# Kernel tuning notes

Hardware: AMD Instinct MI355X
Metric: run time of the kernel (lower is better)

The kernel has to match this reference:

```python
import jax, jax.numpy as jnp
import numpy as np

N_EMBD = 256
N_HEAD = 8
BATCH = 4
SEQ = 2048
NEG_BIAS = -1000000000.0


def setup_inputs() -> dict:
    key = jax.random.key(0)
    ks = jax.random.split(key, 5)
    scale = 1.0 / np.sqrt(N_EMBD)
    x = jax.random.normal(ks[0], (BATCH, SEQ, N_EMBD), dtype=jnp.float32)
    # torch Linear weight layout: (out_features, in_features)
    Wq = jax.random.normal(ks[1], (N_EMBD * N_HEAD, N_EMBD), dtype=jnp.float32) * scale
    Wk = jax.random.normal(ks[2], (N_EMBD * N_HEAD, N_EMBD), dtype=jnp.float32) * scale
    Wv = jax.random.normal(ks[3], (N_EMBD * N_HEAD, N_EMBD), dtype=jnp.float32) * scale
    Wo = jax.random.normal(ks[4], (N_EMBD, N_EMBD * N_HEAD), dtype=jnp.float32) * scale / np.sqrt(N_HEAD)
    return {"x": x, "Wq": Wq, "Wk": Wk, "Wv": Wv, "Wo": Wo}


def reference(x, Wq, Wk, Wv, Wo):
    B, L, E = x.shape
    H, D = N_HEAD, N_EMBD  # d_head == n_embd in this module
    # projections: x @ W.T, then split heads -> (B, H, L, D)
    def proj(W):
        y = jnp.einsum('ble,fe->blf', x, W)  # (B, L, H*D)
        return y.reshape(B, L, H, D).transpose(0, 2, 1, 3)
    q, k, v = proj(Wq), proj(Wk), proj(Wv)
    scores = jnp.einsum('bhld,bhmd->bhlm', q, k) * (E ** -0.5)
    # first (non-causal) softmax over full rows
    attn = jax.nn.softmax(scores, axis=-1)
    # causal mask replaces disallowed probs with large negative bias, then softmax again
    causal = jnp.tril(jnp.ones((L, L), dtype=bool))
    attn = jnp.where(causal[None, None], attn, jnp.asarray(NEG_BIAS, attn.dtype))
    attn = jax.nn.softmax(attn, axis=-1)
    out = jnp.einsum('bhlm,bhmd->bhld', attn, v)  # (B, H, L, D)
    out = out.transpose(0, 2, 1, 3).reshape(B, L, H * D)
    return jnp.einsum('blf,ef->ble', out, Wo)  # (B, L, E)
```

## Files before the change

kernel.cpp:

```cpp
#include <hip/hip_runtime.h>
#include <stdint.h>

typedef unsigned short ushort_t;
typedef __attribute__((ext_vector_type(8))) short bf16x8;
typedef __attribute__((ext_vector_type(4))) float f32x4;
typedef __attribute__((ext_vector_type(4))) unsigned short us4;

#define DEV __device__ __forceinline__

DEV ushort_t f2bf(float f) {
    unsigned int u = __float_as_uint(f);
    u += 0x7fffu + ((u >> 16) & 1u);
    return (ushort_t)(u >> 16);
}

DEV void async16(const ushort_t* g, ushort_t* l) {
    __builtin_amdgcn_global_load_lds(
        (const __attribute__((address_space(1))) void*)g,
        (__attribute__((address_space(3))) void*)l,
        16, 0, 0);
}

__global__ void convert_kernel(const float* __restrict__ x, const float* __restrict__ wq,
                               const float* __restrict__ wk, const float* __restrict__ wv,
                               const float* __restrict__ wo,
                               ushort_t* __restrict__ xb, ushort_t* __restrict__ wqb,
                               ushort_t* __restrict__ wkb, ushort_t* __restrict__ wvb,
                               ushort_t* __restrict__ wob)
{
    const int i = blockIdx.x * 256 + threadIdx.x;
    const float* src; ushort_t* dst; int off;
    if (i < 524288)      { src = x;  dst = xb;  off = i; }
    else if (i < 655360) { src = wq; dst = wqb; off = i - 524288; }
    else if (i < 786432) { src = wk; dst = wkb; off = i - 655360; }
    else if (i < 917504) { src = wv; dst = wvb; off = i - 786432; }
    else                 { src = wo; dst = wob; off = i - 917504; }
    const float4 v = ((const float4*)src)[off];
    us4 o;
    o[0] = f2bf(v.x); o[1] = f2bf(v.y); o[2] = f2bf(v.z); o[3] = f2bf(v.w);
    ((us4*)dst)[off] = o;
}

__global__ __launch_bounds__(256, 2) void qkv_gemm_kernel(
    const ushort_t* __restrict__ A, const ushort_t* __restrict__ wq,
    const ushort_t* __restrict__ wk, const ushort_t* __restrict__ wv,
    ushort_t* __restrict__ q_out, ushort_t* __restrict__ k_out,
    ushort_t* __restrict__ vt_out)
{
    __shared__ ushort_t At[128 * 64];
    __shared__ ushort_t Bt[128 * 64];

    const int K = 256, N = 2048;
    const int z = blockIdx.z;
    const ushort_t* Bm = (z == 0) ? wq : (z == 1) ? wk : wv;

    const int tid  = threadIdx.x;
    const int wave = tid >> 6;
    const int lane = tid & 63;
    const int quad = lane >> 4;
    const int l15  = lane & 15;
    const int mhalf = wave >> 1;
    const int nhalf = wave & 1;
    const int m0 = blockIdx.x * 128;
    const int n0 = blockIdx.y * 128;

    f32x4 acc[4][4];
#pragma unroll
    for (int mf = 0; mf < 4; ++mf)
#pragma unroll
        for (int nf = 0; nf < 4; ++nf)
#pragma unroll
            for (int r = 0; r < 4; ++r) acc[mf][nf][r] = 0.f;

    const int crow = (lane & 7) ^ (lane >> 3);

    for (int k0 = 0; k0 < K; k0 += 64) {
        __syncthreads();
#pragma unroll
        for (int t = 0; t < 4; ++t) {
            const int row = wave * 32 + t * 8 + (lane >> 3);
            async16(A + (size_t)(m0 + row) * K + k0 + crow * 8,
                    At + (wave * 32 + t * 8) * 64 + lane * 8);
            async16(Bm + (size_t)(n0 + row) * K + k0 + crow * 8,
                    Bt + (wave * 32 + t * 8) * 64 + lane * 8);
        }
        __syncthreads();
#pragma unroll
        for (int ks = 0; ks < 2; ++ks) {
            bf16x8 af[4], bf[4];
#pragma unroll
            for (int mf = 0; mf < 4; ++mf) {
                const int ml = mhalf * 64 + mf * 16 + l15;
                const int c = (ks * 4 + quad) ^ (ml & 7);
                af[mf] = *(const bf16x8*)(At + ml * 64 + c * 8);
            }
#pragma unroll
            for (int nf = 0; nf < 4; ++nf) {
                const int nl = nhalf * 64 + nf * 16 + l15;
                const int c = (ks * 4 + quad) ^ (nl & 7);
                bf[nf] = *(const bf16x8*)(Bt + nl * 64 + c * 8);
            }
#pragma unroll
            for (int mf = 0; mf < 4; ++mf)
#pragma unroll
                for (int nf = 0; nf < 4; ++nf)
                    acc[mf][nf] = __builtin_amdgcn_mfma_f32_16x16x32_bf16(
                        af[mf], bf[nf], acc[mf][nf], 0, 0, 0);
        }
    }

    if (z == 2) {
#pragma unroll
        for (int mf = 0; mf < 4; ++mf)
#pragma unroll
            for (int nf = 0; nf < 4; ++nf) {
                const int row = m0 + mhalf * 64 + mf * 16 + quad * 4;
                const int col = n0 + nhalf * 64 + nf * 16 + l15;
                const int b_ = row >> 11, l_ = row & 2047;
                const int h_ = col >> 8, d_ = col & 255;
                us4 pk;
#pragma unroll
                for (int r = 0; r < 4; ++r) pk[r] = f2bf(acc[mf][nf][r]);
                *(us4*)(vt_out + (((size_t)(b_ * 8 + h_) * 256 + d_) * 2048 + l_)) = pk;
            }
    } else {
        ushort_t* Cout = z ? k_out : q_out;
        const float sc = z ? 1.0f : 0.0625f;
#pragma unroll
        for (int mf = 0; mf < 4; ++mf)
#pragma unroll
            for (int nf = 0; nf < 4; ++nf)
#pragma unroll
                for (int r = 0; r < 4; ++r) {
                    const int row = m0 + mhalf * 64 + mf * 16 + quad * 4 + r;
                    const int col = n0 + nhalf * 64 + nf * 16 + l15;
                    Cout[(size_t)row * N + col] = f2bf(acc[mf][nf][r] * sc);
                }
    }
}

__global__ __launch_bounds__(256, 2) void out_gemm_splitk_kernel(
    const ushort_t* __restrict__ A, const ushort_t* __restrict__ Bm,
    float* __restrict__ Pout, int M, int N, int K)
{
    __shared__ ushort_t At[128 * 64];
    __shared__ ushort_t Bt[128 * 64];

    const int tid  = threadIdx.x;
    const int wave = tid >> 6;
    const int lane = tid & 63;
    const int quad = lane >> 4;
    const int l15  = lane & 15;
    const int mhalf = wave >> 1;
    const int nhalf = wave & 1;
    const int m0 = blockIdx.x * 128;
    const int n0 = blockIdx.y * 128;
    const int ks0 = blockIdx.z * 512;

    f32x4 acc[4][4];
#pragma unroll
    for (int mf = 0; mf < 4; ++mf)
#pragma unroll
        for (int nf = 0; nf < 4; ++nf)
#pragma unroll
            for (int r = 0; r < 4; ++r) acc[mf][nf][r] = 0.f;

    const int crow = (lane & 7) ^ (lane >> 3);

    for (int k0 = ks0; k0 < ks0 + 512; k0 += 64) {
        __syncthreads();
#pragma unroll
        for (int t = 0; t < 4; ++t) {
            const int row = wave * 32 + t * 8 + (lane >> 3);
            async16(A + (size_t)(m0 + row) * K + k0 + crow * 8,
                    At + (wave * 32 + t * 8) * 64 + lane * 8);
            async16(Bm + (size_t)(n0 + row) * K + k0 + crow * 8,
                    Bt + (wave * 32 + t * 8) * 64 + lane * 8);
        }
        __syncthreads();
#pragma unroll
        for (int ks = 0; ks < 2; ++ks) {
            bf16x8 af[4], bf[4];
#pragma unroll
            for (int mf = 0; mf < 4; ++mf) {
                const int ml = mhalf * 64 + mf * 16 + l15;
                const int c = (ks * 4 + quad) ^ (ml & 7);
                af[mf] = *(const bf16x8*)(At + ml * 64 + c * 8);
            }
#pragma unroll
            for (int nf = 0; nf < 4; ++nf) {
                const int nl = nhalf * 64 + nf * 16 + l15;
                const int c = (ks * 4 + quad) ^ (nl & 7);
                bf[nf] = *(const bf16x8*)(Bt + nl * 64 + c * 8);
            }
#pragma unroll
            for (int mf = 0; mf < 4; ++mf)
#pragma unroll
                for (int nf = 0; nf < 4; ++nf)
                    acc[mf][nf] = __builtin_amdgcn_mfma_f32_16x16x32_bf16(
                        af[mf], bf[nf], acc[mf][nf], 0, 0, 0);
        }
    }

    float* Cp = Pout + (size_t)blockIdx.z * M * N;
#pragma unroll
    for (int mf = 0; mf < 4; ++mf)
#pragma unroll
        for (int nf = 0; nf < 4; ++nf)
#pragma unroll
            for (int r = 0; r < 4; ++r) {
                const int row = m0 + mhalf * 64 + mf * 16 + quad * 4 + r;
                const int col = n0 + nhalf * 64 + nf * 16 + l15;
                Cp[(size_t)row * N + col] = acc[mf][nf][r];
            }
}

__global__ void reduce4_kernel(const float4* __restrict__ p, float4* __restrict__ out)
{
    const int i = blockIdx.x * 256 + threadIdx.x;
    float4 a = p[i];
    const float4 b = p[i + 524288];
    const float4 c = p[i + 1048576];
    const float4 d = p[i + 1572864];
    a.x += b.x + c.x + d.x;
    a.y += b.y + c.y + d.y;
    a.z += b.z + c.z + d.z;
    a.w += b.w + c.w + d.w;
    out[i] = a;
}

__global__ __launch_bounds__(256, 2) void out_gemm_kernel(
    const ushort_t* __restrict__ A, const ushort_t* __restrict__ Bm,
    float* __restrict__ Cout, int M, int N, int K)
{
    __shared__ ushort_t At[128 * 64];
    __shared__ ushort_t Bt[128 * 64];

    const int tid  = threadIdx.x;
    const int wave = tid >> 6;
    const int lane = tid & 63;
    const int quad = lane >> 4;
    const int l15  = lane & 15;
    const int mhalf = wave >> 1;
    const int nhalf = wave & 1;
    const int m0 = blockIdx.x * 128;
    const int n0 = blockIdx.y * 128;

    f32x4 acc[4][4];
#pragma unroll
    for (int mf = 0; mf < 4; ++mf)
#pragma unroll
        for (int nf = 0; nf < 4; ++nf)
#pragma unroll
            for (int r = 0; r < 4; ++r) acc[mf][nf][r] = 0.f;

    const int crow = (lane & 7) ^ (lane >> 3);

    for (int k0 = 0; k0 < K; k0 += 64) {
        __syncthreads();
#pragma unroll
        for (int t = 0; t < 4; ++t) {
            const int row = wave * 32 + t * 8 + (lane >> 3);
            async16(A + (size_t)(m0 + row) * K + k0 + crow * 8,
                    At + (wave * 32 + t * 8) * 64 + lane * 8);
            async16(Bm + (size_t)(n0 + row) * K + k0 + crow * 8,
                    Bt + (wave * 32 + t * 8) * 64 + lane * 8);
        }
        __syncthreads();
#pragma unroll
        for (int ks = 0; ks < 2; ++ks) {
            bf16x8 af[4], bf[4];
#pragma unroll
            for (int mf = 0; mf < 4; ++mf) {
                const int ml = mhalf * 64 + mf * 16 + l15;
                const int c = (ks * 4 + quad) ^ (ml & 7);
                af[mf] = *(const bf16x8*)(At + ml * 64 + c * 8);
            }
#pragma unroll
            for (int nf = 0; nf < 4; ++nf) {
                const int nl = nhalf * 64 + nf * 16 + l15;
                const int c = (ks * 4 + quad) ^ (nl & 7);
                bf[nf] = *(const bf16x8*)(Bt + nl * 64 + c * 8);
            }
#pragma unroll
            for (int mf = 0; mf < 4; ++mf)
#pragma unroll
                for (int nf = 0; nf < 4; ++nf)
                    acc[mf][nf] = __builtin_amdgcn_mfma_f32_16x16x32_bf16(
                        af[mf], bf[nf], acc[mf][nf], 0, 0, 0);
        }
    }

#pragma unroll
    for (int mf = 0; mf < 4; ++mf)
#pragma unroll
        for (int nf = 0; nf < 4; ++nf)
#pragma unroll
            for (int r = 0; r < 4; ++r) {
                const int row = m0 + mhalf * 64 + mf * 16 + quad * 4 + r;
                const int col = n0 + nhalf * 64 + nf * 16 + l15;
                Cout[(size_t)row * N + col] = acc[mf][nf][r];
            }
}

__global__ __launch_bounds__(512, 4) void pass1_kernel(
    const ushort_t* __restrict__ q_ws, const ushort_t* __restrict__ k_ws,
    float* __restrict__ rz_ws)
{
    __shared__ ushort_t Kt[128 * 256];
    __shared__ float zred[2][128];

    const int tid  = threadIdx.x;
    const int wave = tid >> 6;
    const int lane = tid & 63;
    const int quad = lane >> 4;
    const int l15  = lane & 15;
    const int iq    = wave >> 1;
    const int jhalf = wave & 1;

    const int g  = blockIdx.x;
    const int h  = g & 7;
    const int b  = (g >> 3) & 3;
    const int it = g >> 5;
    const int bh = b * 8 + h;
    const int i0 = it * 128;

    const size_t qkbase = (size_t)b * 2048 * 2048 + (size_t)h * 256;

    bf16x8 qf[2][8];
#pragma unroll
    for (int ng = 0; ng < 2; ++ng) {
        const int i_l = iq * 32 + ng * 16 + l15;
        const ushort_t* qr = q_ws + qkbase + (size_t)(i0 + i_l) * 2048;
#pragma unroll
        for (int ks = 0; ks < 8; ++ks)
            qf[ng][ks] = *(const bf16x8*)(qr + ks * 32 + quad * 8);
    }

    float z[2] = {0.f, 0.f};

    for (int jt = 0; jt < 16; ++jt) {
        __syncthreads();
        {
            const ushort_t* kb = k_ws + qkbase + (size_t)jt * 128 * 2048;
#pragma unroll
            for (int t = 0; t < 8; ++t) {
                const int row = wave * 16 + t * 2 + (lane >> 5);
                const int c = (lane & 31) ^ (row & 7);
                async16(kb + (size_t)row * 2048 + c * 8,
                        Kt + (wave * 16 + t * 2) * 256 + lane * 8);
            }
        }
        __syncthreads();

#pragma unroll
        for (int jh = 0; jh < 2; ++jh) {
            f32x4 sacc[2][2];
#pragma unroll
            for (int a = 0; a < 2; ++a)
#pragma unroll
                for (int c = 0; c < 2; ++c)
#pragma unroll
                    for (int r = 0; r < 4; ++r) sacc[a][c][r] = 0.f;

            __builtin_amdgcn_s_setprio(1);
#pragma unroll
            for (int ks = 0; ks < 8; ++ks) {
                bf16x8 af[2];
#pragma unroll
                for (int mg = 0; mg < 2; ++mg) {
                    const int j_l = jh * 64 + jhalf * 32 + mg * 16 + l15;
                    const int c = (ks * 4 + quad) ^ (j_l & 7);
                    af[mg] = *(const bf16x8*)(Kt + j_l * 256 + c * 8);
                }
#pragma unroll
                for (int mg = 0; mg < 2; ++mg)
#pragma unroll
                    for (int ng = 0; ng < 2; ++ng)
                        sacc[mg][ng] = __builtin_amdgcn_mfma_f32_16x16x32_bf16(
                            af[mg], qf[ng][ks], sacc[mg][ng], 0, 0, 0);
            }
            __builtin_amdgcn_s_setprio(0);

#pragma unroll
            for (int ng = 0; ng < 2; ++ng)
#pragma unroll
                for (int mg = 0; mg < 2; ++mg)
#pragma unroll
                    for (int r = 0; r < 4; ++r)
                        z[ng] += __expf(sacc[mg][ng][r]);
        }
    }

#pragma unroll
    for (int ng = 0; ng < 2; ++ng) {
        z[ng] += __shfl_xor(z[ng], 16);
        z[ng] += __shfl_xor(z[ng], 32);
    }
    __syncthreads();
    if (quad == 0) {
#pragma unroll
        for (int ng = 0; ng < 2; ++ng) {
            const int i_l = iq * 32 + ng * 16 + l15;
            zred[jhalf][i_l] = z[ng];
        }
    }
    __syncthreads();
    if (tid < 128)
        rz_ws[(size_t)bh * 2048 + i0 + tid] = 1.0f / (zred[0][tid] + zred[1][tid]);
}

__global__ __launch_bounds__(512, 2) void pass2_kernel(
    const ushort_t* __restrict__ q_ws, const ushort_t* __restrict__ k_ws,
    const ushort_t* __restrict__ vt_ws, const float* __restrict__ rz_ws,
    ushort_t* __restrict__ attn_out)
{
    __shared__ ushort_t smem[40960];
    ushort_t* Kt = smem;
    ushort_t* Vt = smem + 16384;
    ushort_t* Wt = smem + 32768;

    const int tid  = threadIdx.x;
    const int wave = tid >> 6;
    const int lane = tid & 63;
    const int quad = lane >> 4;
    const int l15  = lane & 15;
    const int iq    = wave >> 1;
    const int jhalf = wave & 1;

    const int g  = blockIdx.x;
    const int h  = g & 7;
    const int b  = (g >> 3) & 3;
    const int x  = g >> 5;
    const int it = (x < 8) ? (2 * x) : (31 - 2 * x);
    const int bh = b * 8 + h;
    const int i0 = it * 128;

    const size_t qkbase = (size_t)b * 2048 * 2048 + (size_t)h * 256;

    bf16x8 qf[2][8];
#pragma unroll
    for (int ng = 0; ng < 2; ++ng) {
        const int i_l = iq * 32 + ng * 16 + l15;
        const ushort_t* qr = q_ws + qkbase + (size_t)(i0 + i_l) * 2048;
#pragma unroll
        for (int ks = 0; ks < 8; ++ks)
            qf[ng][ks] = *(const bf16x8*)(qr + ks * 32 + quad * 8);
    }

    float rzrow[2];
#pragma unroll
    for (int ng = 0; ng < 2; ++ng) {
        const int i_l = iq * 32 + ng * 16 + l15;
        rzrow[ng] = rz_ws[(size_t)bh * 2048 + i0 + i_l];
    }

    f32x4 oacc[2][8];
#pragma unroll
    for (int mg = 0; mg < 2; ++mg)
#pragma unroll
        for (int nf = 0; nf < 8; ++nf)
#pragma unroll
            for (int r = 0; r < 4; ++r) oacc[mg][nf][r] = 0.f;
    float den[2] = {0.f, 0.f};

    const int jmax = 2 * it + 1;
    for (int jt = 0; jt <= jmax; ++jt) {
        const int j0 = jt * 64;
        const int jzone = jt - 2 * it;
        __syncthreads();
        {
            const ushort_t* kb = k_ws + qkbase + (size_t)j0 * 2048;
#pragma unroll
            for (int t = 0; t < 4; ++t) {
                const int row = wave * 8 + t * 2 + (lane >> 5);
                const int c = (lane & 31) ^ (row & 7);
                async16(kb + (size_t)row * 2048 + c * 8,
                        Kt + (wave * 8 + t * 2) * 256 + lane * 8);
            }
            const ushort_t* vb = vt_ws + (size_t)bh * 256 * 2048 + j0;
#pragma unroll
            for (int t = 0; t < 4; ++t) {
                const int row = wave * 32 + t * 8 + (lane >> 3);
                const int c = (lane & 7) ^ (row & 7);
                async16(vb + (size_t)row * 2048 + c * 8,
                        Vt + (wave * 32 + t * 8) * 64 + lane * 8);
            }
        }
        __syncthreads();

        f32x4 sacc[2][2];
#pragma unroll
        for (int a = 0; a < 2; ++a)
#pragma unroll
            for (int c = 0; c < 2; ++c)
#pragma unroll
                for (int r = 0; r < 4; ++r) sacc[a][c][r] = 0.f;

#pragma unroll
        for (int ks = 0; ks < 8; ++ks) {
            bf16x8 af[2];
#pragma unroll
            for (int mg = 0; mg < 2; ++mg) {
                const int j_l = jhalf * 32 + mg * 16 + l15;
                const int c = (ks * 4 + quad) ^ (j_l & 7);
                af[mg] = *(const bf16x8*)(Kt + j_l * 256 + c * 8);
            }
#pragma unroll
            for (int mg = 0; mg < 2; ++mg)
#pragma unroll
                for (int ng = 0; ng < 2; ++ng)
                    sacc[mg][ng] = __builtin_amdgcn_mfma_f32_16x16x32_bf16(
                        af[mg], qf[ng][ks], sacc[mg][ng], 0, 0, 0);
        }

#pragma unroll
        for (int mg = 0; mg < 2; ++mg) {
#pragma unroll
            for (int ng = 0; ng < 2; ++ng) {
                const int i_l = iq * 32 + ng * 16 + l15;
                const int jb = jhalf * 32 + mg * 16 + quad * 4;
                us4 wp;
#pragma unroll
                for (int r = 0; r < 4; ++r) {
                    const float p = __expf(sacc[mg][ng][r]) * rzrow[ng];
                    float w = __expf(p);
                    if (jzone >= 0 && (jzone * 64 + jb + r > i_l)) w = 0.f;
                    den[ng] += w;
                    wp[r] = f2bf(w);
                }
                const int c = (jb >> 3) ^ (i_l & 7);
                *(us4*)(Wt + i_l * 64 + c * 8 + (jb & 7)) = wp;
            }
        }
        __syncthreads();

#pragma unroll
        for (int ks = 0; ks < 2; ++ks) {
            bf16x8 aw[2];
#pragma unroll
            for (int mg = 0; mg < 2; ++mg) {
                const int i_l = iq * 32 + mg * 16 + l15;
                const int c = (ks * 4 + quad) ^ (i_l & 7);
                aw[mg] = *(const bf16x8*)(Wt + i_l * 64 + c * 8);
            }
#pragma unroll
            for (int nf = 0; nf < 8; ++nf) {
                const int d = jhalf * 128 + nf * 16 + l15;
                const int c = (ks * 4 + quad) ^ (d & 7);
                const bf16x8 bv = *(const bf16x8*)(Vt + d * 64 + c * 8);
                oacc[0][nf] = __builtin_amdgcn_mfma_f32_16x16x32_bf16(aw[0], bv, oacc[0][nf], 0, 0, 0);
                oacc[1][nf] = __builtin_amdgcn_mfma_f32_16x16x32_bf16(aw[1], bv, oacc[1][nf], 0, 0, 0);
            }
        }
    }

    __syncthreads();
    {
        float* dbuf = (float*)Kt;
#pragma unroll
        for (int ng = 0; ng < 2; ++ng) {
            const int i_l = iq * 32 + ng * 16 + l15;
            dbuf[(jhalf * 4 + quad) * 128 + i_l] = den[ng];
        }
    }
    __syncthreads();
    if (tid < 128) {
        const float* dbuf = (const float*)Kt;
        float s = 0.f;
#pragma unroll
        for (int p = 0; p < 8; ++p) s += dbuf[p * 128 + tid];
        ((float*)Kt)[1024 + tid] = 1.0f / s;
    }
    __syncthreads();
    {
        const float* rden = (const float*)Kt + 1024;
#pragma unroll
        for (int mg = 0; mg < 2; ++mg) {
#pragma unroll
            for (int r = 0; r < 4; ++r) {
                const int i_l = iq * 32 + mg * 16 + quad * 4 + r;
                const float rd = rden[i_l];
                ushort_t* orow = attn_out + qkbase + (size_t)(i0 + i_l) * 2048;
#pragma unroll
                for (int nf = 0; nf < 8; ++nf) {
                    const int d = jhalf * 128 + nf * 16 + l15;
                    orow[d] = f2bf(oacc[mg][nf][r] * rd);
                }
            }
        }
    }
}

extern "C" void kernel_launch(void* const* d_in, const int* in_sizes, int n_in,
                              void* d_out, int out_size, void* d_ws, size_t ws_size,
                              hipStream_t stream) {
    const float* x  = (const float*)d_in[0];
    const float* Wq = (const float*)d_in[1];
    const float* Wk = (const float*)d_in[2];
    const float* Wv = (const float*)d_in[3];
    const float* Wo = (const float*)d_in[4];

    char* ws = (char*)d_ws;
    ushort_t* xb    = (ushort_t*)(ws);
    ushort_t* wqb   = (ushort_t*)(ws + 4194304);
    ushort_t* wkb   = (ushort_t*)(ws + 5242880);
    ushort_t* wvb   = (ushort_t*)(ws + 6291456);
    ushort_t* wob   = (ushort_t*)(ws + 7340032);
    ushort_t* q_ws  = (ushort_t*)(ws + 8388608);
    ushort_t* k_ws  = (ushort_t*)(ws + 41943040);
    ushort_t* vt_ws = (ushort_t*)(ws + 75497472);
    ushort_t* ao_ws = (ushort_t*)(ws + 109051904);
    float*    rz_ws = (float*)   (ws + 142606336);

    const size_t PG_OFF = 142868480ull;
    const size_t PG_END = PG_OFF + 33554432ull;
    const bool use_splitk = ws_size >= PG_END;
    float* pg_ws = (float*)(ws + PG_OFF);

    convert_kernel<<<4096, 256, 0, stream>>>(x, Wq, Wk, Wv, Wo, xb, wqb, wkb, wvb, wob);

    qkv_gemm_kernel<<<dim3(64, 16, 3), 256, 0, stream>>>(
        xb, wqb, wkb, wvb, q_ws, k_ws, vt_ws);

    pass1_kernel<<<512, 512, 0, stream>>>(q_ws, k_ws, rz_ws);
    pass2_kernel<<<512, 512, 0, stream>>>(q_ws, k_ws, vt_ws, rz_ws, ao_ws);

    if (use_splitk) {
        out_gemm_splitk_kernel<<<dim3(64, 2, 4), 256, 0, stream>>>(
            ao_ws, wob, pg_ws, 8192, 256, 2048);
        reduce4_kernel<<<2048, 256, 0, stream>>>(
            (const float4*)pg_ws, (float4*)d_out);
    } else {
        out_gemm_kernel<<<dim3(64, 2), 256, 0, stream>>>(
            ao_ws, wob, (float*)d_out, 8192, 256, 2048);
    }
}
```

Before: 301.7 us.

## Give each wave full query rows and pass probabilities via shuffles instead of LDS

Pass2 now assigns each wave 16 query rows across the full 64-key tile and the full 256-wide head dimension, replacing the previous 4x2 wave split. The bf16 probability tile is rearranged from the S accumulator layout into the P·V operand layout with cross-lane shuffles, so the Wt LDS buffer, its write/read traffic and one barrier per key tile are gone. The denominator reduction becomes in-wave shuffles rather than an LDS reduction. In exchange each wave holds 16 output accumulators instead of 16 split across two halves, and it reads all of V from LDS, which doubles LDS V reads per wave and adds register pressure.

```diff
diff --git a/kernel.cpp b/kernel.cpp
--- a/kernel.cpp
+++ b/kernel.cpp
@@ -5,6 +5,7 @@
 typedef __attribute__((ext_vector_type(8))) short bf16x8;
 typedef __attribute__((ext_vector_type(4))) float f32x4;
 typedef __attribute__((ext_vector_type(4))) unsigned short us4;
+typedef __attribute__((ext_vector_type(4))) unsigned int u32x4;
 
 #define DEV __device__ __forceinline__
 
@@ -415,18 +416,17 @@
     const ushort_t* __restrict__ vt_ws, const float* __restrict__ rz_ws,
     ushort_t* __restrict__ attn_out)
 {
-    __shared__ ushort_t smem[40960];
+    __shared__ ushort_t smem[32768];
     ushort_t* Kt = smem;
     ushort_t* Vt = smem + 16384;
-    ushort_t* Wt = smem + 32768;
 
     const int tid  = threadIdx.x;
     const int wave = tid >> 6;
     const int lane = tid & 63;
     const int quad = lane >> 4;
     const int l15  = lane & 15;
-    const int iq    = wave >> 1;
-    const int jhalf = wave & 1;
+    const int qlo  = quad & 1;
+    const int qhi  = quad >> 1;
 
     const int g  = blockIdx.x;
     const int h  = g & 7;
@@ -437,32 +437,27 @@
     const int i0 = it * 128;
 
     const size_t qkbase = (size_t)b * 2048 * 2048 + (size_t)h * 256;
-
-    bf16x8 qf[2][8];
-#pragma unroll
-    for (int ng = 0; ng < 2; ++ng) {
-        const int i_l = iq * 32 + ng * 16 + l15;
+    const int i_l = wave * 16 + l15;
+
+    bf16x8 qf[8];
+    {
         const ushort_t* qr = q_ws + qkbase + (size_t)(i0 + i_l) * 2048;
 #pragma unroll
         for (int ks = 0; ks < 8; ++ks)
-            qf[ng][ks] = *(const bf16x8*)(qr + ks * 32 + quad * 8);
-    }
-
-    float rzrow[2];
-#pragma unroll
-    for (int ng = 0; ng < 2; ++ng) {
-        const int i_l = iq * 32 + ng * 16 + l15;
-        rzrow[ng] = rz_ws[(size_t)bh * 2048 + i0 + i_l];
-    }
-
-    f32x4 oacc[2][8];
-#pragma unroll
-    for (int mg = 0; mg < 2; ++mg)
-#pragma unroll
-        for (int nf = 0; nf < 8; ++nf)
-#pragma unroll
-            for (int r = 0; r < 4; ++r) oacc[mg][nf][r] = 0.f;
-    float den[2] = {0.f, 0.f};
+            qf[ks] = *(const bf16x8*)(qr + ks * 32 + quad * 8);
+    }
+
+    const float rzrow = rz_ws[(size_t)bh * 2048 + i0 + i_l];
+
+    f32x4 oacc[16];
+#pragma unroll
+    for (int nf = 0; nf < 16; ++nf)
+#pragma unroll
+        for (int r = 0; r < 4; ++r) oacc[nf][r] = 0.f;
+    float den = 0.f;
+
+    const int srcA = qlo * 32 + l15;
+    const int srcB = srcA + 16;
 
     const int jmax = 2 * it + 1;
     for (int jt = 0; jt <= jmax; ++jt) {
@@ -489,105 +484,91 @@
         }
         __syncthreads();
 
-        f32x4 sacc[2][2];
-#pragma unroll
-        for (int a = 0; a < 2; ++a)
-#pragma unroll
-            for (int c = 0; c < 2; ++c)
-#pragma unroll
-                for (int r = 0; r < 4; ++r) sacc[a][c][r] = 0.f;
+        f32x4 sacc[4];
+#pragma unroll
+        for (int mg = 0; mg < 4; ++mg)
+#pragma unroll
+            for (int r = 0; r < 4; ++r) sacc[mg][r] = 0.f;
 
 #pragma unroll
         for (int ks = 0; ks < 8; ++ks) {
-            bf16x8 af[2];
-#pragma unroll
-            for (int mg = 0; mg < 2; ++mg) {
-                const int j_l = jhalf * 32 + mg * 16 + l15;
+            bf16x8 af[4];
+#pragma unroll
+            for (int mg = 0; mg < 4; ++mg) {
+                const int j_l = mg * 16 + l15;
                 const int c = (ks * 4 + quad) ^ (j_l & 7);
                 af[mg] = *(const bf16x8*)(Kt + j_l * 256 + c * 8);
             }
 #pragma unroll
-            for (int mg = 0; mg < 2; ++mg)
-#pragma unroll
-                for (int ng = 0; ng < 2; ++ng)
-                    sacc[mg][ng] = __builtin_amdgcn_mfma_f32_16x16x32_bf16(
-                        af[mg], qf[ng][ks], sacc[mg][ng], 0, 0, 0);
-        }
-
-#pragma unroll
-        for (int mg = 0; mg < 2; ++mg) {
-#pragma unroll
-            for (int ng = 0; ng < 2; ++ng) {
-                const int i_l = iq * 32 + ng * 16 + l15;
-                const int jb = jhalf * 32 + mg * 16 + quad * 4;
-                us4 wp;
-#pragma unroll
-                for (int r = 0; r < 4; ++r) {
-                    const float p = __expf(sacc[mg][ng][r]) * rzrow[ng];
-                    float w = __expf(p);
-                    if (jzone >= 0 && (jzone * 64 + jb + r > i_l)) w = 0.f;
-                    den[ng] += w;
-                    wp[r] = f2bf(w);
-                }
-                const int c = (jb >> 3) ^ (i_l & 7);
-                *(us4*)(Wt + i_l * 64 + c * 8 + (jb & 7)) = wp;
-            }
-        }
-        __syncthreads();
-
-#pragma unroll
-        for (int ks = 0; ks < 2; ++ks) {
-            bf16x8 aw[2];
-#pragma unroll
-            for (int mg = 0; mg < 2; ++mg) {
-                const int i_l = iq * 32 + mg * 16 + l15;
-                const int c = (ks * 4 + quad) ^ (i_l & 7);
-                aw[mg] = *(const bf16x8*)(Wt + i_l * 64 + c * 8);
-            }
-#pragma unroll
-            for (int nf = 0; nf < 8; ++nf) {
-                const int d = jhalf * 128 + nf * 16 + l15;
-                const int c = (ks * 4 + quad) ^ (d & 7);
+            for (int mg = 0; mg < 4; ++mg)
+                sacc[mg] = __builtin_amdgcn_mfma_f32_16x16x32_bf16(
+                    af[mg], qf[ks], sacc[mg], 0, 0, 0);
+        }
+
+        unsigned int pk[4][2];
+#pragma unroll
+        for (int mg = 0; mg < 4; ++mg) {
+            const int jb = mg * 16 + quad * 4;
+            float wv[4];
+#pragma unroll
+            for (int r = 0; r < 4; ++r) {
+                const float p = __expf(sacc[mg][r]) * rzrow;
+                float w = __expf(p);
+                if (jzone >= 0 && (jzone * 64 + jb + r > i_l)) w = 0.f;
+                den += w;
+                wv[r] = w;
+            }
+            pk[mg][0] = (unsigned int)f2bf(wv[0]) | ((unsigned int)f2bf(wv[1]) << 16);
+            pk[mg][1] = (unsigned int)f2bf(wv[2]) | ((unsigned int)f2bf(wv[3]) << 16);
+        }
+
+        unsigned int sh[4][2][2];
+#pragma unroll
+        for (int mg = 0; mg < 4; ++mg)
+#pragma unroll
+            for (int rp = 0; rp < 2; ++rp) {
+                sh[mg][rp][0] = (unsigned int)__shfl((int)pk[mg][rp], srcA, 64);
+                sh[mg][rp][1] = (unsigned int)__shfl((int)pk[mg][rp], srcB, 64);
+            }
+
+        bf16x8 aw[2];
+#pragma unroll
+        for (int ksp = 0; ksp < 2; ++ksp) {
+            u32x4 t;
+#pragma unroll
+            for (int u = 0; u < 4; ++u) {
+                const unsigned int a0 = sh[ksp * 2][u & 1][u >> 1];
+                const unsigned int a1 = sh[ksp * 2 + 1][u & 1][u >> 1];
+                t[u] = qhi ? a1 : a0;
+            }
+            aw[ksp] = __builtin_bit_cast(bf16x8, t);
+        }
+
+#pragma unroll
+        for (int ksp = 0; ksp < 2; ++ksp)
+#pragma unroll
+            for (int nf = 0; nf < 16; ++nf) {
+                const int d = nf * 16 + l15;
+                const int c = (ksp * 4 + quad) ^ (d & 7);
                 const bf16x8 bv = *(const bf16x8*)(Vt + d * 64 + c * 8);
-                oacc[0][nf] = __builtin_amdgcn_mfma_f32_16x16x32_bf16(aw[0], bv, oacc[0][nf], 0, 0, 0);
-                oacc[1][nf] = __builtin_amdgcn_mfma_f32_16x16x32_bf16(aw[1], bv, oacc[1][nf], 0, 0, 0);
-            }
-        }
-    }
-
-    __syncthreads();
-    {
-        float* dbuf = (float*)Kt;
-#pragma unroll
-        for (int ng = 0; ng < 2; ++ng) {
-            const int i_l = iq * 32 + ng * 16 + l15;
-            dbuf[(jhalf * 4 + quad) * 128 + i_l] = den[ng];
-        }
-    }
-    __syncthreads();
-    if (tid < 128) {
-        const float* dbuf = (const float*)Kt;
-        float s = 0.f;
-#pragma unroll
-        for (int p = 0; p < 8; ++p) s += dbuf[p * 128 + tid];
-        ((float*)Kt)[1024 + tid] = 1.0f / s;
-    }
-    __syncthreads();
-    {
-        const float* rden = (const float*)Kt + 1024;
-#pragma unroll
-        for (int mg = 0; mg < 2; ++mg) {
-#pragma unroll
-            for (int r = 0; r < 4; ++r) {
-                const int i_l = iq * 32 + mg * 16 + quad * 4 + r;
-                const float rd = rden[i_l];
-                ushort_t* orow = attn_out + qkbase + (size_t)(i0 + i_l) * 2048;
-#pragma unroll
-                for (int nf = 0; nf < 8; ++nf) {
-                    const int d = jhalf * 128 + nf * 16 + l15;
-                    orow[d] = f2bf(oacc[mg][nf][r] * rd);
-                }
-            }
+                oacc[nf] = __builtin_amdgcn_mfma_f32_16x16x32_bf16(
+                    aw[ksp], bv, oacc[nf], 0, 0, 0);
+            }
+    }
+
+    den += __shfl_xor(den, 16);
+    den += __shfl_xor(den, 32);
+    const float rdi = 1.0f / den;
+
+#pragma unroll
+    for (int r = 0; r < 4; ++r) {
+        const int io = quad * 4 + r;
+        const float rd = __shfl(rdi, io, 64);
+        ushort_t* orow = attn_out + qkbase + (size_t)(i0 + wave * 16 + io) * 2048;
+#pragma unroll
+        for (int nf = 0; nf < 16; ++nf) {
+            const int d = nf * 16 + l15;
+            orow[d] = f2bf(oacc[nf][r] * rd);
         }
     }
 }
```

After: 328.0 us. 8.7% more time.
